# Performance work log

Hardware: AMD Instinct MI355X
Metric: run time of the kernel (lower is better)

## Reference

```python
import jax, jax.numpy as jnp
import numpy as np

N_NODES = 100000
N_EDGES = 1600000
N_GRAPHS = 4096
IN_DIM, HID, OUT_DIM = 128, 128, 64
BN_EPS = 1e-5


def gcn_conv(x, W, b, src, dst):
    """PyG GCNConv: symmetric norm with self-loops. x:[N,Fin] -> [N,Fout]."""
    h = x @ W  # [N, Fout]
    ones = jnp.ones((src.shape[0],), dtype=h.dtype)
    deg = jax.ops.segment_sum(ones, dst, num_segments=N_NODES) + 1.0  # +1 for self-loop
    dinv = jax.lax.rsqrt(deg)  # deg >= 1, safe
    norm = dinv[src] * dinv[dst]  # [E]
    msg = h[src] * norm[:, None]  # [E, Fout] gather + scale
    agg = jax.ops.segment_sum(msg, dst, num_segments=N_NODES)
    agg = agg + h * (dinv * dinv)[:, None]  # self-loop term, norm = dinv_i^2
    return agg + b


def batchnorm(x, gamma, beta):
    mu = jnp.mean(x, axis=0)
    var = jnp.mean(jnp.square(x - mu), axis=0)  # biased var, torch BN training mode
    return (x - mu) * jax.lax.rsqrt(var + BN_EPS) * gamma + beta


def setup_inputs() -> dict:
    key = jax.random.key(0)
    ks = jax.random.split(key, 12)
    x = jax.random.normal(ks[0], (N_NODES, IN_DIM), dtype=jnp.float32)
    edge_index = jax.random.randint(ks[1], (2, N_EDGES), 0, N_NODES, dtype=jnp.int64)
    batch = jnp.sort(jax.random.randint(ks[2], (N_NODES,), 0, N_GRAPHS, dtype=jnp.int64))
    def lin(k, fi, fo):
        s = 1.0 / np.sqrt(fi)
        return jax.random.uniform(k, (fi, fo), jnp.float32, -s, s)
    return {
        "x": x, "edge_index": edge_index, "batch": batch,
        "W1": lin(ks[3], IN_DIM, HID), "b1": jnp.zeros((HID,), jnp.float32),
        "g1": jnp.ones((HID,), jnp.float32), "be1": jnp.zeros((HID,), jnp.float32),
        "W2": lin(ks[4], HID, HID), "b2": jnp.zeros((HID,), jnp.float32),
        "g2": jnp.ones((HID,), jnp.float32), "be2": jnp.zeros((HID,), jnp.float32),
        "W3": lin(ks[5], HID, HID), "b3": jnp.zeros((HID,), jnp.float32),
        "g3": jnp.ones((HID,), jnp.float32), "be3": jnp.zeros((HID,), jnp.float32),
        "fcW": lin(ks[6], HID, OUT_DIM),
        "fcb": jax.random.uniform(ks[7], (OUT_DIM,), jnp.float32, -1/np.sqrt(HID), 1/np.sqrt(HID)),
    }


def reference(x, edge_index, batch, W1, b1, g1, be1, W2, b2, g2, be2, W3, b3, g3, be3, fcW, fcb):
    src, dst = edge_index[0], edge_index[1]
    h = jax.nn.relu(batchnorm(gcn_conv(x, W1, b1, src, dst), g1, be1))
    h = jax.nn.relu(batchnorm(gcn_conv(h, W2, b2, src, dst), g2, be2))
    h = jax.nn.relu(batchnorm(gcn_conv(h, W3, b3, src, dst), g3, be3))
    # global mean pool over graphs
    sums = jax.ops.segment_sum(h, batch, num_segments=N_GRAPHS)  # [G, HID]
    cnt = jax.ops.segment_sum(jnp.ones((N_NODES,), h.dtype), batch, num_segments=N_GRAPHS)
    pooled = sums / jnp.maximum(cnt, 1.0)[:, None]
    return pooled @ fcW + fcb
```

## Files before the change

kernel.cpp:

```cpp
#include <hip/hip_runtime.h>

#define NN 100000
#define NE 1600000
#define NG 4096
#define HID 128
#define ODIM 64
#define BN_EPS 1e-5f
#define NBUK 782
#define BPAD 896
#define NZROW 256
#define CHUNK 16384
#define PREP_HIST 256
#define PREP_GOFF 17
#define PREP_W 192

typedef unsigned int u32;
typedef unsigned short u16;
typedef short short8 __attribute__((ext_vector_type(8)));
typedef float f32x4 __attribute__((ext_vector_type(4)));

__device__ inline u32 pack_bf16(float a, float b) {
  u32 ua = __float_as_uint(a), ub = __float_as_uint(b);
  ua += 0x7fffu + ((ua >> 16) & 1u);
  ub += 0x7fffu + ((ub >> 16) & 1u);
  return (ua >> 16) | (ub & 0xffff0000u);
}
__device__ inline u16 bf16_of(float v) {
  u32 ua = __float_as_uint(v);
  ua += 0x7fffu + ((ua >> 16) & 1u);
  return (u16)(ua >> 16);
}
__device__ inline float bf_lo(u32 u) { return __uint_as_float(u << 16); }
__device__ inline float bf_hi(u32 u) { return __uint_as_float(u & 0xffff0000u); }

__global__ __launch_bounds__(256) void k_prep(const int* __restrict__ ei, int* __restrict__ bcnt,
                                              const int* __restrict__ batch, int* __restrict__ goff,
                                              const float* __restrict__ W1, const float* __restrict__ W2,
                                              const float* __restrict__ W3, u16* __restrict__ Wt1,
                                              u16* __restrict__ Wt2, u16* __restrict__ Wt3) {
  __shared__ int h[NBUK];
  int b = blockIdx.x, t = threadIdx.x;
  if (b < PREP_HIST) {
    for (int i = t; i < NBUK; i += 256) h[i] = 0;
    __syncthreads();
    const int stride = PREP_HIST * 256;
    for (int e = b * 256 + t; e < NE; e += stride)
      atomicAdd(&h[ei[NE + e] >> 7], 1);
    __syncthreads();
    for (int i = t; i < NBUK; i += 256)
      if (h[i]) atomicAdd(&bcnt[i], h[i]);
  } else if (b < PREP_HIST + PREP_GOFF) {
    int g = (b - PREP_HIST) * 256 + t;
    if (g <= NG) {
      int lo = 0, hi = NN;
      while (lo < hi) { int mid = (lo + hi) >> 1; if (batch[mid] < g) lo = mid + 1; else hi = mid; }
      goff[g] = lo;
    }
  } else {
    int idx = (b - PREP_HIST - PREP_GOFF) * 256 + t;
    int mat = idx >> 14;
    int rem = idx & 16383;
    int n = rem >> 7, k = rem & 127;
    const float* W = (mat == 0) ? W1 : (mat == 1) ? W2 : W3;
    u16* Wt = (mat == 0) ? Wt1 : (mat == 1) ? Wt2 : Wt3;
    Wt[(n << 7) + k] = bf16_of(W[(k << 7) + n]);
  }
}

__global__ __launch_bounds__(1024) void k_bscan(const int* __restrict__ bcnt, int* __restrict__ bboff,
                                                int* __restrict__ bcur) {
  __shared__ int ls[1024];
  int t = threadIdx.x;
  ls[t] = (t < NBUK) ? bcnt[t] : 0;
  __syncthreads();
  for (int d = 1; d < 1024; d <<= 1) {
    int v = 0;
    if (t >= d) v = ls[t - d];
    __syncthreads();
    ls[t] += v;
    __syncthreads();
  }
  if (t < NBUK) {
    int ex = (t == 0) ? 0 : ls[t - 1];
    bboff[t] = ex;
    bcur[t] = ex;
  }
  if (t == 0) bboff[NBUK] = NE;
}

__global__ __launch_bounds__(1024) void k_bscatter(const int* __restrict__ ei, int* __restrict__ bcur,
                                                   u32* __restrict__ ebuf) {
  __shared__ int cnt[NBUK], rnk[NBUK], base[NBUK];
  int t = threadIdx.x;
  int e0 = blockIdx.x * CHUNK;
  for (int i = t; i < NBUK; i += 1024) { cnt[i] = 0; rnk[i] = 0; }
  __syncthreads();
  for (int i = t; i < CHUNK; i += 1024) {
    int e = e0 + i;
    if (e < NE) atomicAdd(&cnt[ei[NE + e] >> 7], 1);
  }
  __syncthreads();
  for (int i = t; i < NBUK; i += 1024) {
    int c = cnt[i];
    base[i] = c ? atomicAdd(&bcur[i], c) : 0;
  }
  __syncthreads();
  for (int i = t; i < CHUNK; i += 1024) {
    int e = e0 + i;
    if (e < NE) {
      int s = ei[e], d = ei[NE + e];
      int b = d >> 7;
      int r = atomicAdd(&rnk[b], 1);
      ebuf[base[b] + r] = ((u32)(d & 127) << 17) | (u32)s;
    }
  }
}

__global__ __launch_bounds__(256) void k_csr(const u32* __restrict__ ebuf, const int* __restrict__ bboff,
                                             int* __restrict__ off, int* __restrict__ oend,
                                             float* __restrict__ dinv, u32* __restrict__ csrc) {
  __shared__ int cnt[128], scn[128], cur[128];
  int b = blockIdx.x, t = threadIdx.x;
  int n0 = b << 7;
  int ebeg = bboff[b], eend = bboff[b + 1];
  int pboff = ebeg + BPAD * b;
  if (t < 128) cnt[t] = 0;
  __syncthreads();
  for (int e = ebeg + t; e < eend; e += 256) atomicAdd(&cnt[ebuf[e] >> 17], 1);
  __syncthreads();
  int pc = 0;
  if (t < 128) { pc = (cnt[t] + 7) & ~7; scn[t] = pc; }
  __syncthreads();
  for (int d = 1; d < 128; d <<= 1) {
    int v = 0;
    if (t >= d && t < 128) v = scn[t - d];
    __syncthreads();
    if (t < 128) scn[t] += v;
    __syncthreads();
  }
  int nvalid = min(128, NN - n0);
  if (t < 128) {
    int ex = scn[t] - pc;
    cur[t] = ex;
    if (t < nvalid) {
      off[n0 + t] = pboff + ex;
      oend[n0 + t] = pboff + scn[t];
      dinv[n0 + t] = rsqrtf((float)cnt[t] + 1.0f);
    }
  }
  __syncthreads();
  for (int e = ebeg + t; e < eend; e += 256) {
    u32 p = ebuf[e];
    int d = p >> 17;
    int pos = pboff + atomicAdd(&cur[d], 1);
    csrc[pos] = (p & 0x1ffffu) << 8;
  }
  if (t < 128) {
    int ex = scn[t] - pc;
    for (int i = cnt[t]; i < pc; ++i)
      csrc[pboff + ex + i] = (u32)(NN + ((n0 + t + i) & (NZROW - 1))) << 8;
  }
}

__global__ __launch_bounds__(256) void k_gemm1(const float* __restrict__ A, const u16* __restrict__ Wt,
                                               const float* __restrict__ dinv, u16* __restrict__ H) {
  __shared__ u16 Ct[128][128];
  u16 (*At)[32] = (u16 (*)[32])(&Ct[0][0]);
  u16 (*Bt)[32] = (u16 (*)[32])(&Ct[32][0]);

  int t = threadIdx.x;
  int w = t >> 6, l = t & 63;
  int quad = l >> 4, lid = l & 15;
  int row0 = blockIdx.x * 128;

  f32x4 acc[2][8];
#pragma unroll
  for (int mt = 0; mt < 2; ++mt)
#pragma unroll
    for (int nt = 0; nt < 8; ++nt) acc[mt][nt] = (f32x4){0.f, 0.f, 0.f, 0.f};

  int ar = t >> 1;
  int ac = (t & 1) << 4;
  int grow = row0 + ar;
  bool aok = grow < NN;

  for (int k0 = 0; k0 < HID; k0 += 32) {
    float4 f0 = {0, 0, 0, 0}, f1 = {0, 0, 0, 0}, f2 = {0, 0, 0, 0}, f3 = {0, 0, 0, 0};
    if (aok) {
      const float4* ap = (const float4*)(A + (size_t)grow * HID + k0 + ac);
      f0 = ap[0]; f1 = ap[1]; f2 = ap[2]; f3 = ap[3];
    }
    uint4 q0, q1;
    q0.x = pack_bf16(f0.x, f0.y); q0.y = pack_bf16(f0.z, f0.w);
    q0.z = pack_bf16(f1.x, f1.y); q0.w = pack_bf16(f1.z, f1.w);
    q1.x = pack_bf16(f2.x, f2.y); q1.y = pack_bf16(f2.z, f2.w);
    q1.z = pack_bf16(f3.x, f3.y); q1.w = pack_bf16(f3.z, f3.w);
    *(uint4*)&At[ar][ac] = q0;
    *(uint4*)&At[ar][ac + 8] = q1;
    const u16* wp = Wt + (size_t)(t >> 1) * HID + k0 + ac;
    *(uint4*)&Bt[t >> 1][ac]     = ((const uint4*)wp)[0];
    *(uint4*)&Bt[t >> 1][ac + 8] = ((const uint4*)wp)[1];
    __syncthreads();
    short8 a0 = *(const short8*)&At[(w << 5) + lid][quad << 3];
    short8 a1 = *(const short8*)&At[(w << 5) + 16 + lid][quad << 3];
#pragma unroll
    for (int nt = 0; nt < 8; ++nt) {
      short8 b = *(const short8*)&Bt[(nt << 4) + lid][quad << 3];
      acc[0][nt] = __builtin_amdgcn_mfma_f32_16x16x32_bf16(a0, b, acc[0][nt], 0, 0, 0);
      acc[1][nt] = __builtin_amdgcn_mfma_f32_16x16x32_bf16(a1, b, acc[1][nt], 0, 0, 0);
    }
    __syncthreads();
  }

  int valid = min(128, NN - row0);
#pragma unroll
  for (int mt = 0; mt < 2; ++mt) {
#pragma unroll
    for (int r = 0; r < 4; ++r) {
      int rl = (w << 5) + (mt << 4) + (quad << 2) + r;
      float dv = (rl < valid) ? dinv[row0 + rl] : 0.f;
#pragma unroll
      for (int nt = 0; nt < 8; ++nt) {
        Ct[rl][(nt << 4) + lid] = bf16_of(acc[mt][nt][r] * dv);
      }
    }
  }
  __syncthreads();
  u16* Hb = H + (size_t)row0 * HID;
  int tot = valid << 4;
  for (int idx = t; idx < tot; idx += 256) {
    ((uint4*)Hb)[idx] = ((const uint4*)Ct)[idx];
  }
}

__device__ inline u32 bn_pair(u32 v, float2 sc, float2 sh) {
  float a = fmaxf(fmaf(bf_lo(v), sc.x, sh.x), 0.f);
  float b = fmaxf(fmaf(bf_hi(v), sc.y, sh.y), 0.f);
  return pack_bf16(a, b);
}

__global__ __launch_bounds__(256) void k_gemm_b(const u16* __restrict__ A, const u16* __restrict__ Wt,
                                                const float* __restrict__ sums, const float* __restrict__ g,
                                                const float* __restrict__ be,
                                                const float* __restrict__ dinv, u16* __restrict__ H) {
  __shared__ u16 Ct[128][128];
  u16 (*At)[32] = (u16 (*)[32])(&Ct[0][0]);
  u16 (*Bt)[32] = (u16 (*)[32])(&Ct[32][0]);
  float* scsh = (float*)&Ct[64][0];

  int t = threadIdx.x;
  int w = t >> 6, l = t & 63;
  int quad = l >> 4, lid = l & 15;
  int row0 = blockIdx.x * 128;

  if (t < 128) {
    const float invN = 1.0f / (float)NN;
    float mu = sums[t] * invN;
    float var = sums[HID + t] * invN - mu * mu;
    float sc = g[t] * rsqrtf(var + BN_EPS);
    scsh[t] = sc;
    scsh[128 + t] = be[t] - mu * sc;
  }

  f32x4 acc[2][8];
#pragma unroll
  for (int mt = 0; mt < 2; ++mt)
#pragma unroll
    for (int nt = 0; nt < 8; ++nt) acc[mt][nt] = (f32x4){0.f, 0.f, 0.f, 0.f};

  int ar = t >> 1;
  int ac = (t & 1) << 4;
  int grow = row0 + ar;
  bool aok = grow < NN;
  __syncthreads();

  for (int k0 = 0; k0 < HID; k0 += 32) {
    uint4 q0 = {0, 0, 0, 0}, q1 = {0, 0, 0, 0};
    if (aok) {
      const uint4* ap = (const uint4*)(A + (size_t)grow * HID + k0 + ac);
      q0 = ap[0]; q1 = ap[1];
    }
    const float2* scp = (const float2*)(scsh + k0 + ac);
    const float2* shp = (const float2*)(scsh + 128 + k0 + ac);
    q0.x = bn_pair(q0.x, scp[0], shp[0]); q0.y = bn_pair(q0.y, scp[1], shp[1]);
    q0.z = bn_pair(q0.z, scp[2], shp[2]); q0.w = bn_pair(q0.w, scp[3], shp[3]);
    q1.x = bn_pair(q1.x, scp[4], shp[4]); q1.y = bn_pair(q1.y, scp[5], shp[5]);
    q1.z = bn_pair(q1.z, scp[6], shp[6]); q1.w = bn_pair(q1.w, scp[7], shp[7]);
    *(uint4*)&At[ar][ac] = q0;
    *(uint4*)&At[ar][ac + 8] = q1;
    const u16* wp = Wt + (size_t)(t >> 1) * HID + k0 + ac;
    *(uint4*)&Bt[t >> 1][ac]     = ((const uint4*)wp)[0];
    *(uint4*)&Bt[t >> 1][ac + 8] = ((const uint4*)wp)[1];
    __syncthreads();
    short8 a0 = *(const short8*)&At[(w << 5) + lid][quad << 3];
    short8 a1 = *(const short8*)&At[(w << 5) + 16 + lid][quad << 3];
#pragma unroll
    for (int nt = 0; nt < 8; ++nt) {
      short8 b = *(const short8*)&Bt[(nt << 4) + lid][quad << 3];
      acc[0][nt] = __builtin_amdgcn_mfma_f32_16x16x32_bf16(a0, b, acc[0][nt], 0, 0, 0);
      acc[1][nt] = __builtin_amdgcn_mfma_f32_16x16x32_bf16(a1, b, acc[1][nt], 0, 0, 0);
    }
    __syncthreads();
  }

  int valid = min(128, NN - row0);
#pragma unroll
  for (int mt = 0; mt < 2; ++mt) {
#pragma unroll
    for (int r = 0; r < 4; ++r) {
      int rl = (w << 5) + (mt << 4) + (quad << 2) + r;
      float dv = (rl < valid) ? dinv[row0 + rl] : 0.f;
#pragma unroll
      for (int nt = 0; nt < 8; ++nt) {
        Ct[rl][(nt << 4) + lid] = bf16_of(acc[mt][nt][r] * dv);
      }
    }
  }
  __syncthreads();
  u16* Hb = H + (size_t)row0 * HID;
  int tot = valid << 4;
  for (int idx = t; idx < tot; idx += 256) {
    ((uint4*)Hb)[idx] = ((const uint4*)Ct)[idx];
  }
}

__global__ __launch_bounds__(256) void k_agg(const u16* __restrict__ h2, const int* __restrict__ off,
                                             const int* __restrict__ oend, const u32* __restrict__ csrc,
                                             const float* __restrict__ dinv, u16* __restrict__ aggb) {
  int node = (int)((blockIdx.x * 256 + threadIdx.x) >> 6);
  int lane = threadIdx.x & 63;
  if (node >= NN) return;
  int half = lane >> 5;
  u32 lb8 = (u32)(lane & 31) << 3;
  const char* h2b = (const char*)h2;
  int beg = off[node], end = oend[node];
  float f0 = 0.f, f1 = 0.f, f2 = 0.f, f3 = 0.f;
  if (half == 0) {
    uint2 us = *(const uint2*)(h2b + (((size_t)node << 8) + lb8));
    f0 = bf_lo(us.x); f1 = bf_hi(us.x); f2 = bf_lo(us.y); f3 = bf_hi(us.y);
  }
  int e = beg;
  for (; e + 16 <= end; e += 16) {
    u32 s[8]; uint2 v[8];
#pragma unroll
    for (int i = 0; i < 8; ++i) s[i] = csrc[e + 2 * i + half];
#pragma unroll
    for (int i = 0; i < 8; ++i) v[i] = *(const uint2*)(h2b + ((size_t)s[i] + lb8));
#pragma unroll
    for (int i = 0; i < 8; ++i) {
      f0 += bf_lo(v[i].x); f1 += bf_hi(v[i].x);
      f2 += bf_lo(v[i].y); f3 += bf_hi(v[i].y);
    }
  }
  if (e < end) {
    u32 s[4]; uint2 v[4];
#pragma unroll
    for (int i = 0; i < 4; ++i) s[i] = csrc[e + 2 * i + half];
#pragma unroll
    for (int i = 0; i < 4; ++i) v[i] = *(const uint2*)(h2b + ((size_t)s[i] + lb8));
#pragma unroll
    for (int i = 0; i < 4; ++i) {
      f0 += bf_lo(v[i].x); f1 += bf_hi(v[i].x);
      f2 += bf_lo(v[i].y); f3 += bf_hi(v[i].y);
    }
  }
  f0 += __shfl_xor(f0, 32, 64);
  f1 += __shfl_xor(f1, 32, 64);
  f2 += __shfl_xor(f2, 32, 64);
  f3 += __shfl_xor(f3, 32, 64);
  if (half == 0) {
    float di = dinv[node];
    uint2 p;
    p.x = pack_bf16(f0 * di, f1 * di);
    p.y = pack_bf16(f2 * di, f3 * di);
    *(uint2*)((char*)aggb + (((size_t)node << 8) + lb8)) = p;
  }
}

__global__ __launch_bounds__(256) void k_bnstats(const u16* __restrict__ X, float* __restrict__ buf) {
  __shared__ float lsx[256], lssx[256], lsy[256], lssy[256];
  int t = threadIdx.x;
  int colp = t & 63, grp = t >> 6;
  int rbeg = blockIdx.x * 256, rend = min(rbeg + 256, NN);
  float sx = 0.f, ssx = 0.f, sy = 0.f, ssy = 0.f;
  for (int r = rbeg + grp; r < rend; r += 4) {
    u32 v = ((const u32*)(X + (size_t)r * HID))[colp];
    float a = bf_lo(v), b = bf_hi(v);
    sx += a; ssx = fmaf(a, a, ssx);
    sy += b; ssy = fmaf(b, b, ssy);
  }
  lsx[t] = sx; lssx[t] = ssx; lsy[t] = sy; lssy[t] = ssy;
  __syncthreads();
  if (t < 64) {
    sx = lsx[t] + lsx[t + 64] + lsx[t + 128] + lsx[t + 192];
    ssx = lssx[t] + lssx[t + 64] + lssx[t + 128] + lssx[t + 192];
    sy = lsy[t] + lsy[t + 64] + lsy[t + 128] + lsy[t + 192];
    ssy = lssy[t] + lssy[t + 64] + lssy[t + 128] + lssy[t + 192];
    atomicAdd(&buf[2 * colp], sx);
    atomicAdd(&buf[2 * colp + 1], sy);
    atomicAdd(&buf[HID + 2 * colp], ssx);
    atomicAdd(&buf[HID + 2 * colp + 1], ssy);
  }
}

__global__ __launch_bounds__(256) void k_poolfc(const u16* __restrict__ aggb, const float* __restrict__ sums,
                                                const float* __restrict__ g3, const float* __restrict__ be3,
                                                const int* __restrict__ goff, const float* __restrict__ fcW,
                                                const float* __restrict__ fcb, float* __restrict__ out) {
  __shared__ float ls[4][128];
  int t = threadIdx.x;
  int w = t >> 6, lane = t & 63;
  int gr = blockIdx.x * 4 + w;
  const float invN = 1.0f / (float)NN;
  int f0 = lane << 1, f1 = f0 + 1;
  float mu0 = sums[f0] * invN, mu1 = sums[f1] * invN;
  float v0 = sums[HID + f0] * invN - mu0 * mu0;
  float v1 = sums[HID + f1] * invN - mu1 * mu1;
  float sc0 = g3[f0] * rsqrtf(v0 + BN_EPS), sc1 = g3[f1] * rsqrtf(v1 + BN_EPS);
  float sh0 = be3[f0] - mu0 * sc0, sh1 = be3[f1] - mu1 * sc1;
  int beg = goff[gr], end = goff[gr + 1];
  float ax = 0.f, ay = 0.f;
  for (int r = beg; r < end; ++r) {
    u32 v = ((const u32*)(aggb + (size_t)r * HID))[lane];
    ax += fmaxf(fmaf(bf_lo(v), sc0, sh0), 0.f);
    ay += fmaxf(fmaf(bf_hi(v), sc1, sh1), 0.f);
  }
  float inv = 1.0f / fmaxf((float)(end - beg), 1.0f);
  ls[w][f0] = ax * inv;
  ls[w][f1] = ay * inv;
  __syncthreads();
  float acc = fcb[lane];
#pragma unroll 8
  for (int k = 0; k < HID; ++k) acc = fmaf(ls[w][k], fcW[(size_t)k * ODIM + lane], acc);
  out[(size_t)gr * ODIM + lane] = acc;
}

extern "C" void kernel_launch(void* const* d_in, const int* in_sizes, int n_in,
                              void* d_out, int out_size, void* d_ws, size_t ws_size,
                              hipStream_t stream) {
  const float* x     = (const float*)d_in[0];
  const int*   ei    = (const int*)d_in[1];
  const int*   batch = (const int*)d_in[2];
  const float* W1    = (const float*)d_in[3];
  const float* g1    = (const float*)d_in[5];
  const float* be1   = (const float*)d_in[6];
  const float* W2    = (const float*)d_in[7];
  const float* g2    = (const float*)d_in[9];
  const float* be2   = (const float*)d_in[10];
  const float* W3    = (const float*)d_in[11];
  const float* g3    = (const float*)d_in[13];
  const float* be3   = (const float*)d_in[14];
  const float* fcW   = (const float*)d_in[15];
  const float* fcb   = (const float*)d_in[16];
  float* out = (float*)d_out;

  char* p = (char*)d_ws;
  auto alloc = [&](size_t bytes) { char* r = p; p += (bytes + 255) & ~(size_t)255; return r; };
  int*   bcnt   = (int*)alloc((size_t)NBUK * 4);
  float* bnb    = (float*)alloc(3 * 256 * 4);
  size_t zbytes = (size_t)(p - (char*)d_ws);
  int*   bboff  = (int*)alloc((size_t)(NBUK + 1) * 4);
  int*   bcur   = (int*)alloc((size_t)NBUK * 4);
  int*   off    = (int*)alloc((size_t)NN * 4);
  int*   oend   = (int*)alloc((size_t)NN * 4);
  float* dinv   = (float*)alloc((size_t)NN * 4);
  u32*   ebuf   = (u32*)alloc((size_t)NE * 4);
  u32*   csrc   = (u32*)alloc(((size_t)NE + (size_t)BPAD * NBUK) * 4);
  int*   goff   = (int*)alloc((size_t)(NG + 1) * 4);
  u16*   Wt1    = (u16*)alloc((size_t)HID * HID * 2);
  u16*   Wt2    = (u16*)alloc((size_t)HID * HID * 2);
  u16*   Wt3    = (u16*)alloc((size_t)HID * HID * 2);
  u16*   h2     = (u16*)alloc((size_t)(NN + NZROW) * HID * 2);
  u16*   aggb   = (u16*)alloc((size_t)NN * HID * 2);

  hipMemsetAsync(d_ws, 0, zbytes, stream);
  hipMemsetAsync(h2 + (size_t)NN * HID, 0, (size_t)NZROW * HID * 2, stream);

  const int NB = (NN + 255) / 256;
  const int GB = (NN + 127) / 128;
  const int AGB = NN / 4;
  const int SB = (NE + CHUNK - 1) / CHUNK;

  k_prep<<<PREP_HIST + PREP_GOFF + PREP_W, 256, 0, stream>>>(ei, bcnt, batch, goff, W1, W2, W3, Wt1, Wt2, Wt3);
  k_bscan<<<1, 1024, 0, stream>>>(bcnt, bboff, bcur);
  k_bscatter<<<SB, 1024, 0, stream>>>(ei, bcur, ebuf);
  k_csr<<<NBUK, 256, 0, stream>>>(ebuf, bboff, off, oend, dinv, csrc);

  k_gemm1<<<GB, 256, 0, stream>>>(x, Wt1, dinv, h2);
  k_agg<<<AGB, 256, 0, stream>>>(h2, off, oend, csrc, dinv, aggb);
  k_bnstats<<<NB, 256, 0, stream>>>(aggb, bnb);
  k_gemm_b<<<GB, 256, 0, stream>>>(aggb, Wt2, bnb, g1, be1, dinv, h2);
  k_agg<<<AGB, 256, 0, stream>>>(h2, off, oend, csrc, dinv, aggb);
  k_bnstats<<<NB, 256, 0, stream>>>(aggb, bnb + 256);
  k_gemm_b<<<GB, 256, 0, stream>>>(aggb, Wt3, bnb + 256, g2, be2, dinv, h2);
  k_agg<<<AGB, 256, 0, stream>>>(h2, off, oend, csrc, dinv, aggb);
  k_bnstats<<<NB, 256, 0, stream>>>(aggb, bnb + 512);
  k_poolfc<<<NG / 4, 256, 0, stream>>>(aggb, bnb + 512, g3, be3, goff, fcW, fcb, out);
}
```

Measured before the change: 522.4 us.

## Load GEMM operands directly into MFMA registers, dropping LDS staging and barriers

Both GEMM kernels now load each wave's A fragments and the bf16 weight fragments straight from global memory into the register layout the MFMA expects, instead of staging tiles through shared memory with two barriers per k-step. This removes the LDS round trips and the per-iteration __syncthreads. The cost is that weight loads are repeated across waves and blocks (served from cache), and global accesses become 16-byte strided reads rather than cooperative coalesced tile loads. k_gemm_b now keeps its BN scale/shift in a separate shared array.

```diff
diff --git a/kernel.cpp b/kernel.cpp
--- a/kernel.cpp
+++ b/kernel.cpp
@@ -165,9 +165,6 @@
 __global__ __launch_bounds__(256) void k_gemm1(const float* __restrict__ A, const u16* __restrict__ Wt,
                                                const float* __restrict__ dinv, u16* __restrict__ H) {
   __shared__ u16 Ct[128][128];
-  u16 (*At)[32] = (u16 (*)[32])(&Ct[0][0]);
-  u16 (*Bt)[32] = (u16 (*)[32])(&Ct[32][0]);
-
   int t = threadIdx.x;
   int w = t >> 6, l = t & 63;
   int quad = l >> 4, lid = l & 15;
@@ -179,37 +176,36 @@
 #pragma unroll
     for (int nt = 0; nt < 8; ++nt) acc[mt][nt] = (f32x4){0.f, 0.f, 0.f, 0.f};
 
-  int ar = t >> 1;
-  int ac = (t & 1) << 4;
-  int grow = row0 + ar;
-  bool aok = grow < NN;
+  int ra0 = row0 + (w << 5) + lid;
+  int ra1 = ra0 + 16;
+  bool ok0 = ra0 < NN, ok1 = ra1 < NN;
+  int cb = quad << 3;
 
   for (int k0 = 0; k0 < HID; k0 += 32) {
     float4 f0 = {0, 0, 0, 0}, f1 = {0, 0, 0, 0}, f2 = {0, 0, 0, 0}, f3 = {0, 0, 0, 0};
-    if (aok) {
-      const float4* ap = (const float4*)(A + (size_t)grow * HID + k0 + ac);
-      f0 = ap[0]; f1 = ap[1]; f2 = ap[2]; f3 = ap[3];
-    }
-    uint4 q0, q1;
-    q0.x = pack_bf16(f0.x, f0.y); q0.y = pack_bf16(f0.z, f0.w);
-    q0.z = pack_bf16(f1.x, f1.y); q0.w = pack_bf16(f1.z, f1.w);
-    q1.x = pack_bf16(f2.x, f2.y); q1.y = pack_bf16(f2.z, f2.w);
-    q1.z = pack_bf16(f3.x, f3.y); q1.w = pack_bf16(f3.z, f3.w);
-    *(uint4*)&At[ar][ac] = q0;
-    *(uint4*)&At[ar][ac + 8] = q1;
-    const u16* wp = Wt + (size_t)(t >> 1) * HID + k0 + ac;
-    *(uint4*)&Bt[t >> 1][ac]     = ((const uint4*)wp)[0];
-    *(uint4*)&Bt[t >> 1][ac + 8] = ((const uint4*)wp)[1];
-    __syncthreads();
-    short8 a0 = *(const short8*)&At[(w << 5) + lid][quad << 3];
-    short8 a1 = *(const short8*)&At[(w << 5) + 16 + lid][quad << 3];
+    if (ok0) {
+      const float4* ap = (const float4*)(A + (size_t)ra0 * HID + k0 + cb);
+      f0 = ap[0]; f1 = ap[1];
+    }
+    if (ok1) {
+      const float4* ap = (const float4*)(A + (size_t)ra1 * HID + k0 + cb);
+      f2 = ap[0]; f3 = ap[1];
+    }
+    uint4 ua, ub;
+    ua.x = pack_bf16(f0.x, f0.y); ua.y = pack_bf16(f0.z, f0.w);
+    ua.z = pack_bf16(f1.x, f1.y); ua.w = pack_bf16(f1.z, f1.w);
+    ub.x = pack_bf16(f2.x, f2.y); ub.y = pack_bf16(f2.z, f2.w);
+    ub.z = pack_bf16(f3.x, f3.y); ub.w = pack_bf16(f3.z, f3.w);
+    short8 a0, a1;
+    *(uint4*)&a0 = ua;
+    *(uint4*)&a1 = ub;
+    const u16* wb = Wt + (size_t)lid * HID + k0 + cb;
 #pragma unroll
     for (int nt = 0; nt < 8; ++nt) {
-      short8 b = *(const short8*)&Bt[(nt << 4) + lid][quad << 3];
+      short8 b = *(const short8*)(wb + (size_t)(nt << 4) * HID);
       acc[0][nt] = __builtin_amdgcn_mfma_f32_16x16x32_bf16(a0, b, acc[0][nt], 0, 0, 0);
       acc[1][nt] = __builtin_amdgcn_mfma_f32_16x16x32_bf16(a1, b, acc[1][nt], 0, 0, 0);
     }
-    __syncthreads();
   }
 
   int valid = min(128, NN - row0);
@@ -244,10 +240,7 @@
                                                 const float* __restrict__ be,
                                                 const float* __restrict__ dinv, u16* __restrict__ H) {
   __shared__ u16 Ct[128][128];
-  u16 (*At)[32] = (u16 (*)[32])(&Ct[0][0]);
-  u16 (*Bt)[32] = (u16 (*)[32])(&Ct[32][0]);
-  float* scsh = (float*)&Ct[64][0];
-
+  __shared__ float scsh[256];
   int t = threadIdx.x;
   int w = t >> 6, l = t & 63;
   int quad = l >> 4, lid = l & 15;
@@ -268,39 +261,34 @@
 #pragma unroll
     for (int nt = 0; nt < 8; ++nt) acc[mt][nt] = (f32x4){0.f, 0.f, 0.f, 0.f};
 
-  int ar = t >> 1;
-  int ac = (t & 1) << 4;
-  int grow = row0 + ar;
-  bool aok = grow < NN;
+  int ra0 = row0 + (w << 5) + lid;
+  int ra1 = ra0 + 16;
+  bool ok0 = ra0 < NN, ok1 = ra1 < NN;
+  int cb = quad << 3;
   __syncthreads();
 
   for (int k0 = 0; k0 < HID; k0 += 32) {
-    uint4 q0 = {0, 0, 0, 0}, q1 = {0, 0, 0, 0};
-    if (aok) {
-      const uint4* ap = (const uint4*)(A + (size_t)grow * HID + k0 + ac);
-      q0 = ap[0]; q1 = ap[1];
-    }
-    const float2* scp = (const float2*)(scsh + k0 + ac);
-    const float2* shp = (const float2*)(scsh + 128 + k0 + ac);
-    q0.x = bn_pair(q0.x, scp[0], shp[0]); q0.y = bn_pair(q0.y, scp[1], shp[1]);
-    q0.z = bn_pair(q0.z, scp[2], shp[2]); q0.w = bn_pair(q0.w, scp[3], shp[3]);
-    q1.x = bn_pair(q1.x, scp[4], shp[4]); q1.y = bn_pair(q1.y, scp[5], shp[5]);
-    q1.z = bn_pair(q1.z, scp[6], shp[6]); q1.w = bn_pair(q1.w, scp[7], shp[7]);
-    *(uint4*)&At[ar][ac] = q0;
-    *(uint4*)&At[ar][ac + 8] = q1;
-    const u16* wp = Wt + (size_t)(t >> 1) * HID + k0 + ac;
-    *(uint4*)&Bt[t >> 1][ac]     = ((const uint4*)wp)[0];
-    *(uint4*)&Bt[t >> 1][ac + 8] = ((const uint4*)wp)[1];
-    __syncthreads();
-    short8 a0 = *(const short8*)&At[(w << 5) + lid][quad << 3];
-    short8 a1 = *(const short8*)&At[(w << 5) + 16 + lid][quad << 3];
+    uint4 qa = {0, 0, 0, 0}, qb = {0, 0, 0, 0};
+    if (ok0) qa = *(const uint4*)(A + (size_t)ra0 * HID + k0 + cb);
+    if (ok1) qb = *(const uint4*)(A + (size_t)ra1 * HID + k0 + cb);
+    const float2* scp = (const float2*)(scsh + k0 + cb);
+    const float2* shp = (const float2*)(scsh + 128 + k0 + cb);
+    float2 s0 = scp[0], s1 = scp[1], s2 = scp[2], s3 = scp[3];
+    float2 h0 = shp[0], h1 = shp[1], h2 = shp[2], h3 = shp[3];
+    qa.x = bn_pair(qa.x, s0, h0); qa.y = bn_pair(qa.y, s1, h1);
+    qa.z = bn_pair(qa.z, s2, h2); qa.w = bn_pair(qa.w, s3, h3);
+    qb.x = bn_pair(qb.x, s0, h0); qb.y = bn_pair(qb.y, s1, h1);
+    qb.z = bn_pair(qb.z, s2, h2); qb.w = bn_pair(qb.w, s3, h3);
+    short8 a0, a1;
+    *(uint4*)&a0 = qa;
+    *(uint4*)&a1 = qb;
+    const u16* wb = Wt + (size_t)lid * HID + k0 + cb;
 #pragma unroll
     for (int nt = 0; nt < 8; ++nt) {
-      short8 b = *(const short8*)&Bt[(nt << 4) + lid][quad << 3];
+      short8 b = *(const short8*)(wb + (size_t)(nt << 4) * HID);
       acc[0][nt] = __builtin_amdgcn_mfma_f32_16x16x32_bf16(a0, b, acc[0][nt], 0, 0, 0);
       acc[1][nt] = __builtin_amdgcn_mfma_f32_16x16x32_bf16(a1, b, acc[1][nt], 0, 0, 0);
     }
-    __syncthreads();
   }
 
   int valid = min(128, NN - row0);
```

Result: slower. 551.5 us (+5.6%).
